# Performance work log

Measured on AMD Instinct MI355X. Metric: run time of the kernel, lower is better.

## Reference

```python
import jax, jax.numpy as jnp
import numpy as np

B, T, C = 1, 3072, 1024
H, KVH, HD = 16, 4, 64
HI, DI = 16, 32
LOCAL = 128
TOP_K = max(int(T * 0.5), LOCAL)  # 1536
EPS = 1.1920929e-07  # torch fp32 finfo eps used by F.rms_norm
NEG = -1.0e9
POS = 1.0e9


def _rope(x, cos, sin):
    d = x.shape[-1] // 2
    x1, x2 = x[..., :d], x[..., d:]
    return jnp.concatenate([x1 * cos + x2 * sin, -x1 * sin + x2 * cos], axis=-1)


def _rms(x):
    return x * jax.lax.rsqrt(jnp.mean(x * x, axis=-1, keepdims=True) + EPS)


def setup_inputs() -> dict:
    key = jax.random.key(0)
    ks = jax.random.split(key, 10)
    s = 0.02
    return {
        "x": jax.random.normal(ks[0], (B, T, C), jnp.float32),
        "cos": jax.random.uniform(ks[1], (1, T, 1, HD // 2), jnp.float32),
        "sin": jax.random.uniform(ks[2], (1, T, 1, HD // 2), jnp.float32),
        "Wq": jax.random.normal(ks[3], (C, H * HD), jnp.float32) * s,
        "Wk": jax.random.normal(ks[4], (C, KVH * HD), jnp.float32) * s,
        "Wv": jax.random.normal(ks[5], (C, KVH * HD), jnp.float32) * s,
        "Wo": jax.random.normal(ks[6], (C, C), jnp.float32) * s,
        "Wiq": jax.random.normal(ks[7], (C, HI * DI), jnp.float32) * s,
        "Wik": jax.random.normal(ks[8], (C, DI), jnp.float32) * s,
        "Wiw": jax.random.normal(ks[9], (C, HI), jnp.float32) * s,
    }


def reference(x, cos, sin, Wq, Wk, Wv, Wo, Wiq, Wik, Wiw):
    # projections
    q = (x @ Wq).reshape(B, T, H, HD)
    k = (x @ Wk).reshape(B, T, KVH, HD)
    v = (x @ Wv).reshape(B, T, KVH, HD)
    q, k = _rope(q, cos, sin), _rope(k, cos, sin)
    q, k = _rms(q), _rms(k)

    # lightning indexer: I(t,s) = sum_h w(t,h) * relu(q_I(t,h).k_I(s))
    iq = (x @ Wiq).reshape(B, T, HI, DI)
    ik = x @ Wik  # (B,T,DI)
    iw = x @ Wiw  # (B,T,HI)
    sc = jax.nn.relu(jnp.einsum('bqhd,bkd->bqhk', iq, ik))
    imp = jnp.einsum('bqh,bqhk->bqk', iw, sc)  # (B,T,T)

    pos = jnp.arange(T)
    causal = (pos[None, :] > pos[:, None])  # True where key s > query t
    dist = pos[None, :] - pos[:, None]
    in_local = (dist >= 0) & (dist < LOCAL)
    imp = jnp.where(causal[None], NEG, imp)
    imp = jnp.where(in_local[None], POS, imp)

    # hard top-k mask
    _, top_idx = jax.lax.top_k(imp, TOP_K)  # (B,T,K)
    bi = jnp.arange(B)[:, None, None]
    ti = jnp.arange(T)[None, :, None]
    hard = jnp.zeros((B, T, T), x.dtype).at[bi, ti, top_idx].set(1.0)
    causal_f = causal.astype(x.dtype)[None]
    hard = hard * (1.0 - causal_f)
    di = jnp.arange(T)
    hard = hard.at[:, di, di].set(1.0)

    # straight-through sigmoid gate
    soft = jax.nn.sigmoid(imp * 0.1) * (1.0 - causal_f)
    soft = soft.at[:, di, di].set(1.0)
    gate = soft + jax.lax.stop_gradient(hard - soft)
    attn_bias = jnp.log(jnp.clip(gate, 1e-6))[:, None]  # (B,1,T,T)

    # GQA attention with additive bias
    rep = H // KVH
    qs = q.transpose(0, 2, 1, 3)                        # (B,H,T,HD)
    ks_ = jnp.repeat(k.transpose(0, 2, 1, 3), rep, axis=1)
    vs = jnp.repeat(v.transpose(0, 2, 1, 3), rep, axis=1)
    scale = 1.0 / np.sqrt(HD)
    logits = jnp.einsum('bhqd,bhkd->bhqk', qs, ks_) * scale + attn_bias
    att = jax.nn.softmax(logits, axis=-1)
    y = jnp.einsum('bhqk,bhkd->bhqd', att, vs)
    y = y.transpose(0, 2, 1, 3).reshape(B, T, C)
    return y @ Wo
```

## Files before the change

kernel.cpp:

```cpp
#include <hip/hip_runtime.h>
#include <hip/hip_bf16.h>
#include <math.h>

#define T_SEQ   3072
#define C_DIM   1024
#define NH      16
#define NKV     4
#define HD      64
#define HI      16
#define DI      32
#define LOCAL_W 128
#define TOPK    1536
#define SELQ0   (TOPK - LOCAL_W + 1)
#define RMS_EPS 1.1920929e-07f
#define LOGEPS  -13.815510558f
#define SCALE   0.125f
#define MASKW   (T_SEQ / 32)
#define QKVI_N  2176
#define IQ_OFF  1536
#define IK_OFF  2048
#define IW_OFF  2080

typedef __bf16 bf16_t;
typedef __bf16 bf16x8 __attribute__((ext_vector_type(8)));
typedef float  f32x4  __attribute__((ext_vector_type(4)));

__global__ __launch_bounds__(256) void transp_conv(const float* __restrict__ W,
                                                   bf16_t* __restrict__ Wt, int N) {
    __shared__ float t[64][65];
    int n0 = blockIdx.x * 64, k0 = blockIdx.y * 64;
#pragma unroll
    for (int it = 0; it < 16; ++it) {
        int flat = it * 256 + threadIdx.x;
        int i = flat >> 6, j = flat & 63;
        t[i][j] = W[(size_t)(k0 + i) * N + n0 + j];
    }
    __syncthreads();
#pragma unroll
    for (int it = 0; it < 16; ++it) {
        int flat = it * 256 + threadIdx.x;
        int n = flat >> 6, kk = flat & 63;
        Wt[(size_t)(n0 + n) * 1024 + k0 + kk] = (bf16_t)t[kk][n];
    }
}

__global__ __launch_bounds__(256) void transp_conv_g(const float* __restrict__ W,
                                                     bf16_t* __restrict__ Wt, int N) {
    __shared__ float t[64][65];
    int k0 = blockIdx.y * 64;
#pragma unroll
    for (int it = 0; it < 16; ++it) {
        int flat = it * 256 + threadIdx.x;
        int i = flat >> 6, j = flat & 63;
        t[i][j] = (j < N) ? W[(size_t)(k0 + i) * N + j] : 0.f;
    }
    __syncthreads();
#pragma unroll
    for (int it = 0; it < 16; ++it) {
        int flat = it * 256 + threadIdx.x;
        int n = flat >> 6, kk = flat & 63;
        if (n < N) Wt[(size_t)n * 1024 + k0 + kk] = (bf16_t)t[kk][n];
    }
}

__global__ __launch_bounds__(256) void pack_kv(const float* __restrict__ qkvi,
                                               bf16_t* __restrict__ Kb,
                                               bf16_t* __restrict__ Vtg) {
    __shared__ float t[64][65];
    int t0 = blockIdx.x * 64, kvh = blockIdx.y;
#pragma unroll
    for (int it = 0; it < 2; ++it) {
        int s = it * 256 + threadIdx.x;
        int row = s >> 3, slot = s & 7;
        const float* src = &qkvi[(size_t)(t0 + row) * QKVI_N + 1024 + kvh * HD + slot * 8];
        float4 a = *reinterpret_cast<const float4*>(src);
        float4 b = *reinterpret_cast<const float4*>(src + 4);
        bf16x8 v;
        v[0] = (bf16_t)a.x; v[1] = (bf16_t)a.y; v[2] = (bf16_t)a.z; v[3] = (bf16_t)a.w;
        v[4] = (bf16_t)b.x; v[5] = (bf16_t)b.y; v[6] = (bf16_t)b.z; v[7] = (bf16_t)b.w;
        *reinterpret_cast<bf16x8*>(&Kb[(size_t)(t0 + row) * (NKV * HD) + kvh * HD + slot * 8]) = v;
    }
#pragma unroll
    for (int it = 0; it < 16; ++it) {
        int flat = it * 256 + threadIdx.x;
        int i = flat >> 6, j = flat & 63;
        t[i][j] = qkvi[(size_t)(t0 + i) * QKVI_N + 1280 + kvh * HD + j];
    }
    __syncthreads();
#pragma unroll
    for (int it = 0; it < 16; ++it) {
        int flat = it * 256 + threadIdx.x;
        int dd = flat >> 6, tt = flat & 63;
        Vtg[(size_t)(kvh * HD + dd) * T_SEQ + t0 + tt] = (bf16_t)t[tt][dd];
    }
}

__global__ __launch_bounds__(256) void causal_mask(unsigned* __restrict__ selm) {
    int idx = blockIdx.x * 256 + threadIdx.x;
    if (idx >= SELQ0 * MASKW) return;
    int row = idx / MASKW, w = idx % MASKW;
    int wq = row >> 5, b = row & 31;
    unsigned v;
    if (w < wq) v = ~0u;
    else if (w == wq) v = (b == 31) ? ~0u : ((1u << (b + 1)) - 1u);
    else v = 0u;
    selm[(size_t)row * MASKW + w] = v;
}

template<bool A_F32>
__global__ __launch_bounds__(256) void gemm_mfma_t(const void* __restrict__ Ap,
                                                   const bf16_t* __restrict__ Bt,
                                                   float* __restrict__ C, int N) {
    __shared__ __align__(16) bf16_t As[128 * 64];
    __shared__ __align__(16) bf16_t Bs[128 * 64];
    const int tid = threadIdx.x;
    const int m0 = blockIdx.y * 128, n0 = blockIdx.x * 128;
    const int wid = tid >> 6, lane = tid & 63;
    const int wr = wid >> 1, wc = wid & 1;
    const int fr = lane & 15, fq = lane >> 4;

    f32x4 acc[4][4];
#pragma unroll
    for (int i = 0; i < 4; ++i)
#pragma unroll
        for (int j = 0; j < 4; ++j) acc[i][j] = (f32x4){0.f, 0.f, 0.f, 0.f};

    for (int k0 = 0; k0 < 1024; k0 += 64) {
        __syncthreads();
#pragma unroll
        for (int s = tid; s < 1024; s += 256) {
            int row = s >> 3, slot = s & 7;
            int sw = slot ^ (row & 7);
            bf16x8 av;
            if constexpr (A_F32) {
                const float* A = (const float*)Ap;
                const float* src = &A[(size_t)(m0 + row) * 1024 + k0 + slot * 8];
                float4 a = *reinterpret_cast<const float4*>(src);
                float4 b = *reinterpret_cast<const float4*>(src + 4);
                av[0] = (bf16_t)a.x; av[1] = (bf16_t)a.y; av[2] = (bf16_t)a.z; av[3] = (bf16_t)a.w;
                av[4] = (bf16_t)b.x; av[5] = (bf16_t)b.y; av[6] = (bf16_t)b.z; av[7] = (bf16_t)b.w;
            } else {
                const bf16_t* A = (const bf16_t*)Ap;
                av = *reinterpret_cast<const bf16x8*>(&A[(size_t)(m0 + row) * 1024 + k0 + slot * 8]);
            }
            *reinterpret_cast<bf16x8*>(&As[row * 64 + sw * 8]) = av;
            bf16x8 bv = *reinterpret_cast<const bf16x8*>(&Bt[(size_t)(n0 + row) * 1024 + k0 + slot * 8]);
            *reinterpret_cast<bf16x8*>(&Bs[row * 64 + sw * 8]) = bv;
        }
        __syncthreads();
#pragma unroll
        for (int kk = 0; kk < 2; ++kk) {
            bf16x8 af[4], bfr[4];
#pragma unroll
            for (int i = 0; i < 4; ++i) {
                int arow = wr * 64 + i * 16 + fr;
                int aslot = (kk * 4 + fq) ^ (arow & 7);
                af[i] = *reinterpret_cast<const bf16x8*>(&As[arow * 64 + aslot * 8]);
                int brow = wc * 64 + i * 16 + fr;
                int bslot = (kk * 4 + fq) ^ (brow & 7);
                bfr[i] = *reinterpret_cast<const bf16x8*>(&Bs[brow * 64 + bslot * 8]);
            }
#pragma unroll
            for (int i = 0; i < 4; ++i)
#pragma unroll
                for (int j = 0; j < 4; ++j)
                    acc[i][j] = __builtin_amdgcn_mfma_f32_16x16x32_bf16(af[i], bfr[j], acc[i][j], 0, 0, 0);
        }
    }
#pragma unroll
    for (int i = 0; i < 4; ++i)
#pragma unroll
        for (int j = 0; j < 4; ++j)
#pragma unroll
            for (int r = 0; r < 4; ++r) {
                int row = m0 + wr * 64 + i * 16 + fq * 4 + r;
                int col = n0 + wc * 64 + j * 16 + fr;
                C[(size_t)row * N + col] = acc[i][j][r];
            }
}

__global__ __launch_bounds__(256) void rope_rms(float* __restrict__ data,
                                                const float* __restrict__ cosb,
                                                const float* __restrict__ sinb,
                                                int nheads, int rowstride, int coloff) {
    int idx = blockIdx.x * blockDim.x + threadIdx.x;
    if (idx >= T_SEQ * nheads) return;
    int t = idx / nheads, hh = idx % nheads;
    float* p = data + (size_t)t * rowstride + coloff + hh * HD;
    float o[HD];
    float ss = 0.f;
#pragma unroll
    for (int d = 0; d < 32; ++d) {
        float x1 = p[d], x2 = p[d + 32];
        float c = cosb[t * 32 + d], s = sinb[t * 32 + d];
        float a = x1 * c + x2 * s;
        float b = x2 * c - x1 * s;
        o[d] = a; o[d + 32] = b;
        ss += a * a + b * b;
    }
    float r = 1.0f / sqrtf(ss * (1.0f / HD) + RMS_EPS);
#pragma unroll
    for (int d = 0; d < HD; ++d) p[d] = o[d] * r;
}

__global__ __launch_bounds__(256) void imp_select(const float* __restrict__ qkvi,
                                                  unsigned* __restrict__ selmask) {
    const int q = SELQ0 + blockIdx.x;
    const int tid = threadIdx.x;
    const int wid = tid >> 6, lane = tid & 63;
    const int fr = lane & 15, fq = lane >> 4;

    __shared__ unsigned keys[T_SEQ];
    __shared__ unsigned hist[256];
    __shared__ int sufx[257];
    __shared__ unsigned gtw[MASKW], eqw[MASKW];
    __shared__ int s_digit, s_need;

    const float* iqp = &qkvi[(size_t)q * QKVI_N + IQ_OFF + fr * DI + fq * 8];
    float4 qa = *reinterpret_cast<const float4*>(iqp);
    float4 qb = *reinterpret_cast<const float4*>(iqp + 4);
    bf16x8 bq;
    bq[0] = (bf16_t)qa.x; bq[1] = (bf16_t)qa.y; bq[2] = (bf16_t)qa.z; bq[3] = (bf16_t)qa.w;
    bq[4] = (bf16_t)qb.x; bq[5] = (bf16_t)qb.y; bq[6] = (bf16_t)qb.z; bq[7] = (bf16_t)qb.w;
    const float wh = qkvi[(size_t)q * QKVI_N + IW_OFF + fr];

    for (int k0 = 0; k0 < q; k0 += 64) {
        int krow = k0 + wid * 16 + fr;
        const float* ikp = &qkvi[(size_t)krow * QKVI_N + IK_OFF + fq * 8];
        float4 a = *reinterpret_cast<const float4*>(ikp);
        float4 b = *reinterpret_cast<const float4*>(ikp + 4);
        bf16x8 ak;
        ak[0] = (bf16_t)a.x; ak[1] = (bf16_t)a.y; ak[2] = (bf16_t)a.z; ak[3] = (bf16_t)a.w;
        ak[4] = (bf16_t)b.x; ak[5] = (bf16_t)b.y; ak[6] = (bf16_t)b.z; ak[7] = (bf16_t)b.w;
        f32x4 c = (f32x4){0.f, 0.f, 0.f, 0.f};
        c = __builtin_amdgcn_mfma_f32_16x16x32_bf16(ak, bq, c, 0, 0, 0);
        float p0 = wh * fmaxf(c[0], 0.f);
        float p1 = wh * fmaxf(c[1], 0.f);
        float p2 = wh * fmaxf(c[2], 0.f);
        float p3 = wh * fmaxf(c[3], 0.f);
#pragma unroll
        for (int m = 1; m < 16; m <<= 1) {
            p0 += __shfl_xor(p0, m);
            p1 += __shfl_xor(p1, m);
            p2 += __shfl_xor(p2, m);
            p3 += __shfl_xor(p3, m);
        }
        if (fr == 0) {
            int kb = k0 + wid * 16 + fq * 4;
            float pv[4] = {p0, p1, p2, p3};
#pragma unroll
            for (int r = 0; r < 4; ++r) {
                int k = kb + r;
                if (k < q) {
                    unsigned u = __float_as_uint(pv[r]);
                    keys[k] = (u & 0x80000000u) ? ~u : (u | 0x80000000u);
                }
            }
        }
    }
    __syncthreads();

    const int F = min(LOCAL_W, T_SEQ - q);
    int need = TOPK - F;
    unsigned pref = 0;
    for (int b = 3; b >= 0; --b) {
        hist[tid] = 0;
        __syncthreads();
        unsigned above = (b == 3) ? 0u : (~0u << ((b + 1) * 8));
        for (int k = tid; k < q; k += 256) {
            unsigned key = keys[k];
            if ((key & above) == (pref & above))
                atomicAdd(&hist[(key >> (b * 8)) & 255u], 1u);
        }
        __syncthreads();
        sufx[tid] = (int)hist[tid];
        if (tid == 0) sufx[256] = 0;
        __syncthreads();
        for (int s = 1; s < 256; s <<= 1) {
            int v = sufx[tid] + ((tid + s < 256) ? sufx[tid + s] : 0);
            __syncthreads();
            sufx[tid] = v;
            __syncthreads();
        }
        int nxt = sufx[tid + 1];
        if (sufx[tid] >= need && nxt < need) { s_digit = tid; s_need = need - nxt; }
        __syncthreads();
        pref |= ((unsigned)s_digit) << (b * 8);
        need = s_need;
        __syncthreads();
    }
    const unsigned V = pref;
    const int slots = need;

    for (int w = tid; w < MASKW; w += 256) {
        unsigned g = 0, e = 0;
        int kbase = w * 32;
#pragma unroll 4
        for (int bit = 0; bit < 32; ++bit) {
            int k = kbase + bit;
            if (k < q) {
                unsigned key = keys[k];
                if (key > V) g |= (1u << bit);
                else if (key == V) e |= (1u << bit);
            }
        }
        gtw[w] = g; eqw[w] = e;
    }
    __syncthreads();
    if (tid == 0) {
        int rem = slots;
        for (int w = 0; w < MASKW && rem > 0; ++w) {
            unsigned e = eqw[w];
            if (!e) continue;
            int pc = __popc(e);
            if (pc <= rem) { gtw[w] |= e; rem -= pc; }
            else {
                unsigned sel = 0;
                for (int i = 0; i < rem; ++i) { unsigned lb = e & (~e + 1u); sel |= lb; e ^= lb; }
                gtw[w] |= sel; rem = 0;
            }
        }
    }
    __syncthreads();
    for (int w = tid; w < MASKW; w += 256) {
        unsigned g = gtw[w];
        if (w == (q >> 5)) g |= (1u << (q & 31));
        selmask[(size_t)q * MASKW + w] = g;
    }
}

__global__ __launch_bounds__(256) void attn_mfma(const float* __restrict__ qkvi,
                                                 const bf16_t* __restrict__ Kb,
                                                 const bf16_t* __restrict__ Vtg,
                                                 const unsigned* __restrict__ selmask,
                                                 float* __restrict__ yb) {
    const int q0 = blockIdx.x * 64;
    const int h = blockIdx.y;
    const int kvh = h >> 2;
    const int tid = threadIdx.x;
    const int wid = tid >> 6, lane = tid & 63;
    const int fr = lane & 15, fq = lane >> 4;

    __shared__ __align__(16) bf16_t Qs[64 * 64];
    __shared__ __align__(16) bf16_t Ks[64 * 64];
    __shared__ __align__(16) bf16_t Vts[64 * 64];
    __shared__ __align__(16) float Sb[64][68];
    __shared__ unsigned mlds[64][2];
    __shared__ float mrow[64], lrow[64], arow[64];

#pragma unroll
    for (int it = 0; it < 2; ++it) {
        int s = it * 256 + tid;
        int row = s >> 3, slot = s & 7;
        const float* src = &qkvi[(size_t)(q0 + row) * QKVI_N + h * HD + slot * 8];
        float4 a = *reinterpret_cast<const float4*>(src);
        float4 b = *reinterpret_cast<const float4*>(src + 4);
        bf16x8 v;
        v[0] = (bf16_t)(a.x * SCALE); v[1] = (bf16_t)(a.y * SCALE);
        v[2] = (bf16_t)(a.z * SCALE); v[3] = (bf16_t)(a.w * SCALE);
        v[4] = (bf16_t)(b.x * SCALE); v[5] = (bf16_t)(b.y * SCALE);
        v[6] = (bf16_t)(b.z * SCALE); v[7] = (bf16_t)(b.w * SCALE);
        *reinterpret_cast<bf16x8*>(&Qs[row * 64 + (slot ^ (row & 7)) * 8]) = v;
    }
    if (tid < 64) { mrow[tid] = -1e30f; lrow[tid] = 0.f; }

    f32x4 oc[4];
#pragma unroll
    for (int j = 0; j < 4; ++j) oc[j] = (f32x4){0.f, 0.f, 0.f, 0.f};
    __syncthreads();

    for (int k0 = 0; k0 < T_SEQ; k0 += 64) {
#pragma unroll
        for (int it = 0; it < 2; ++it) {
            int s = it * 256 + tid;
            int row = s >> 3, slot = s & 7;
            *reinterpret_cast<bf16x8*>(&Ks[row * 64 + (slot ^ (row & 7)) * 8]) =
                *reinterpret_cast<const bf16x8*>(&Kb[(size_t)(k0 + row) * (NKV * HD) + kvh * HD + slot * 8]);
            *reinterpret_cast<bf16x8*>(&Vts[row * 64 + (slot ^ (row & 7)) * 8]) =
                *reinterpret_cast<const bf16x8*>(&Vtg[(size_t)(kvh * HD + row) * T_SEQ + k0 + slot * 8]);
        }
        if (tid < 128) {
            int row = tid >> 1, w = tid & 1;
            mlds[row][w] = selmask[(size_t)(q0 + row) * MASKW + (k0 >> 5) + w];
        }
        __syncthreads();

        f32x4 sacc[4];
#pragma unroll
        for (int j = 0; j < 4; ++j) sacc[j] = (f32x4){0.f, 0.f, 0.f, 0.f};
#pragma unroll
        for (int kc = 0; kc < 2; ++kc) {
            int arow_ = wid * 16 + fr;
            bf16x8 aq = *reinterpret_cast<const bf16x8*>(&Qs[arow_ * 64 + (((kc * 4 + fq) ^ (arow_ & 7))) * 8]);
#pragma unroll
            for (int jb = 0; jb < 4; ++jb) {
                int brow = jb * 16 + fr;
                bf16x8 bk = *reinterpret_cast<const bf16x8*>(&Ks[brow * 64 + (((kc * 4 + fq) ^ (brow & 7))) * 8]);
                sacc[jb] = __builtin_amdgcn_mfma_f32_16x16x32_bf16(aq, bk, sacc[jb], 0, 0, 0);
            }
        }
#pragma unroll
        for (int jb = 0; jb < 4; ++jb)
#pragma unroll
            for (int r = 0; r < 4; ++r) {
                unsigned mw = mlds[wid * 16 + fq * 4 + r][jb >> 1];
                float bias = ((mw >> ((jb & 1) * 16 + fr)) & 1u) ? 0.f : LOGEPS;
                Sb[wid * 16 + fq * 4 + r][jb * 16 + fr] = sacc[jb][r] + bias;
            }
        __syncthreads();

        {
            int r = tid >> 2, ln = tid & 3;
            float4* sp = reinterpret_cast<float4*>(&Sb[r][ln * 16]);
            float4 v0 = sp[0], v1 = sp[1], v2 = sp[2], v3 = sp[3];
            float mx = fmaxf(fmaxf(fmaxf(v0.x, v0.y), fmaxf(v0.z, v0.w)),
                             fmaxf(fmaxf(v1.x, v1.y), fmaxf(v1.z, v1.w)));
            mx = fmaxf(mx, fmaxf(fmaxf(fmaxf(v2.x, v2.y), fmaxf(v2.z, v2.w)),
                                 fmaxf(fmaxf(v3.x, v3.y), fmaxf(v3.z, v3.w))));
            mx = fmaxf(mx, __shfl_xor(mx, 1, 64));
            mx = fmaxf(mx, __shfl_xor(mx, 2, 64));
            float mnew = fmaxf(mrow[r], mx);
            v0.x = __expf(v0.x - mnew); v0.y = __expf(v0.y - mnew);
            v0.z = __expf(v0.z - mnew); v0.w = __expf(v0.w - mnew);
            v1.x = __expf(v1.x - mnew); v1.y = __expf(v1.y - mnew);
            v1.z = __expf(v1.z - mnew); v1.w = __expf(v1.w - mnew);
            v2.x = __expf(v2.x - mnew); v2.y = __expf(v2.y - mnew);
            v2.z = __expf(v2.z - mnew); v2.w = __expf(v2.w - mnew);
            v3.x = __expf(v3.x - mnew); v3.y = __expf(v3.y - mnew);
            v3.z = __expf(v3.z - mnew); v3.w = __expf(v3.w - mnew);
            float ssum = (v0.x + v0.y + v0.z + v0.w) + (v1.x + v1.y + v1.z + v1.w)
                       + (v2.x + v2.y + v2.z + v2.w) + (v3.x + v3.y + v3.z + v3.w);
            sp[0] = v0; sp[1] = v1; sp[2] = v2; sp[3] = v3;
            ssum += __shfl_xor(ssum, 1, 64);
            ssum += __shfl_xor(ssum, 2, 64);
            if (ln == 0) {
                float a = __expf(mrow[r] - mnew);
                lrow[r] = lrow[r] * a + ssum;
                mrow[r] = mnew;
                arow[r] = a;
            }
        }
        __syncthreads();

#pragma unroll
        for (int r = 0; r < 4; ++r) {
            float a = arow[wid * 16 + fq * 4 + r];
#pragma unroll
            for (int jb = 0; jb < 4; ++jb) oc[jb][r] *= a;
        }
#pragma unroll
        for (int kc = 0; kc < 2; ++kc) {
            const float* ps = &Sb[wid * 16 + fr][kc * 32 + fq * 8];
            float4 p0 = *reinterpret_cast<const float4*>(ps);
            float4 p1 = *reinterpret_cast<const float4*>(ps + 4);
            bf16x8 ap;
            ap[0] = (bf16_t)p0.x; ap[1] = (bf16_t)p0.y; ap[2] = (bf16_t)p0.z; ap[3] = (bf16_t)p0.w;
            ap[4] = (bf16_t)p1.x; ap[5] = (bf16_t)p1.y; ap[6] = (bf16_t)p1.z; ap[7] = (bf16_t)p1.w;
#pragma unroll
            for (int jb = 0; jb < 4; ++jb) {
                int brow = jb * 16 + fr;
                bf16x8 bv = *reinterpret_cast<const bf16x8*>(&Vts[brow * 64 + (((kc * 4 + fq) ^ (brow & 7))) * 8]);
                oc[jb] = __builtin_amdgcn_mfma_f32_16x16x32_bf16(ap, bv, oc[jb], 0, 0, 0);
            }
        }
        __syncthreads();
    }

#pragma unroll
    for (int r = 0; r < 4; ++r) {
        int rowl = wid * 16 + fq * 4 + r;
        float inv = 1.0f / lrow[rowl];
#pragma unroll
        for (int jb = 0; jb < 4; ++jb)
            yb[(size_t)(q0 + rowl) * C_DIM + h * HD + jb * 16 + fr] = oc[jb][r] * inv;
    }
}

extern "C" void kernel_launch(void* const* d_in, const int* in_sizes, int n_in,
                              void* d_out, int out_size, void* d_ws, size_t ws_size,
                              hipStream_t stream) {
    const float* x    = (const float*)d_in[0];
    const float* cosb = (const float*)d_in[1];
    const float* sinb = (const float*)d_in[2];
    const float* Wq   = (const float*)d_in[3];
    const float* Wk   = (const float*)d_in[4];
    const float* Wv   = (const float*)d_in[5];
    const float* Wo   = (const float*)d_in[6];
    const float* Wiq  = (const float*)d_in[7];
    const float* Wik  = (const float*)d_in[8];
    const float* Wiw  = (const float*)d_in[9];
    float* out = (float*)d_out;

    char* cur = (char*)d_ws;
    auto carve = [&](size_t bytes) { char* p = cur; cur += (bytes + 255) & ~(size_t)255; return p; };
    float*    qkvi  = (float*)   carve((size_t)T_SEQ * QKVI_N * 4);
    float*    yb    = (float*)   carve((size_t)T_SEQ * C_DIM * 4);
    unsigned* selm  = (unsigned*)carve((size_t)T_SEQ * MASKW * 4);
    bf16_t*   Wtp   = (bf16_t*)  carve((size_t)QKVI_N * C_DIM * 2);
    bf16_t*   Wot   = (bf16_t*)  carve((size_t)C_DIM * C_DIM * 2);
    bf16_t*   Vtg   = (bf16_t*)  carve((size_t)NKV * HD * T_SEQ * 2);
    bf16_t*   Kb16  = (bf16_t*)  carve((size_t)T_SEQ * NKV * HD * 2);
    if ((size_t)(cur - (char*)d_ws) > ws_size) return;

    dim3 blk(256);

    transp_conv<<<dim3(16, 16), blk, 0, stream>>>(Wq,  Wtp + (size_t)0    * 1024, 1024);
    transp_conv<<<dim3(4, 16),  blk, 0, stream>>>(Wk,  Wtp + (size_t)1024 * 1024, 256);
    transp_conv<<<dim3(4, 16),  blk, 0, stream>>>(Wv,  Wtp + (size_t)1280 * 1024, 256);
    transp_conv<<<dim3(8, 16),  blk, 0, stream>>>(Wiq, Wtp + (size_t)IQ_OFF * 1024, 512);
    transp_conv_g<<<dim3(1, 16), blk, 0, stream>>>(Wik, Wtp + (size_t)IK_OFF * 1024, DI);
    transp_conv_g<<<dim3(1, 16), blk, 0, stream>>>(Wiw, Wtp + (size_t)IW_OFF * 1024, HI);
    transp_conv<<<dim3(16, 16), blk, 0, stream>>>(Wo,  Wot, 1024);

    gemm_mfma_t<true><<<dim3(QKVI_N / 128, T_SEQ / 128), blk, 0, stream>>>(x, Wtp, qkvi, QKVI_N);
    causal_mask<<<(SELQ0 * MASKW + 255) / 256, blk, 0, stream>>>(selm);

    rope_rms<<<(T_SEQ * NH + 255) / 256, blk, 0, stream>>>(qkvi, cosb, sinb, NH, QKVI_N, 0);
    rope_rms<<<(T_SEQ * NKV + 255) / 256, blk, 0, stream>>>(qkvi, cosb, sinb, NKV, QKVI_N, 1024);
    pack_kv<<<dim3(T_SEQ / 64, NKV), blk, 0, stream>>>(qkvi, Kb16, Vtg);

    imp_select<<<T_SEQ - SELQ0, blk, 0, stream>>>(qkvi, selm);

    attn_mfma<<<dim3(T_SEQ / 64, NH), blk, 0, stream>>>(qkvi, Kb16, Vtg, selm, yb);

    gemm_mfma_t<true><<<dim3(C_DIM / 128, T_SEQ / 128), blk, 0, stream>>>(yb, Wot, out, C_DIM);
}
```

Measured before the change: 429.7 us.

## Keep attention softmax in registers via transposed S=K·Q MFMA and lane shuffles

The attention kernel now computes scores as K·Q so each lane holds all keys for one query row, which lets it do the online-softmax max and sum in registers with cross-lane shuffles. The shared-memory score buffer, the Q staging buffer, the per-row m/l/alpha arrays and two of the three barriers per tile are removed. The probabilities are packed to bf16 and redistributed with shuffles into the A-operand layout for the P·V MFMA. This adds shuffle traffic and register pressure in exchange for less LDS traffic and fewer synchronisations.

New measurement: 419.6 us. 1.02x faster.

```diff
diff --git a/kernel.cpp b/kernel.cpp
--- a/kernel.cpp
+++ b/kernel.cpp
@@ -25,6 +25,12 @@
 typedef __bf16 bf16x8 __attribute__((ext_vector_type(8)));
 typedef float  f32x4  __attribute__((ext_vector_type(4)));
 
+static __device__ inline unsigned packbf(float a, float b) {
+    union { bf16_t h[2]; unsigned u; } cv;
+    cv.h[0] = (bf16_t)a; cv.h[1] = (bf16_t)b;
+    return cv.u;
+}
+
 __global__ __launch_bounds__(256) void transp_conv(const float* __restrict__ W,
                                                    bf16_t* __restrict__ Wt, int N) {
     __shared__ float t[64][65];
@@ -341,35 +347,33 @@
     const int wid = tid >> 6, lane = tid & 63;
     const int fr = lane & 15, fq = lane >> 4;
 
-    __shared__ __align__(16) bf16_t Qs[64 * 64];
     __shared__ __align__(16) bf16_t Ks[64 * 64];
     __shared__ __align__(16) bf16_t Vts[64 * 64];
-    __shared__ __align__(16) float Sb[64][68];
     __shared__ unsigned mlds[64][2];
-    __shared__ float mrow[64], lrow[64], arow[64];
-
-#pragma unroll
-    for (int it = 0; it < 2; ++it) {
-        int s = it * 256 + tid;
-        int row = s >> 3, slot = s & 7;
-        const float* src = &qkvi[(size_t)(q0 + row) * QKVI_N + h * HD + slot * 8];
-        float4 a = *reinterpret_cast<const float4*>(src);
-        float4 b = *reinterpret_cast<const float4*>(src + 4);
-        bf16x8 v;
-        v[0] = (bf16_t)(a.x * SCALE); v[1] = (bf16_t)(a.y * SCALE);
-        v[2] = (bf16_t)(a.z * SCALE); v[3] = (bf16_t)(a.w * SCALE);
-        v[4] = (bf16_t)(b.x * SCALE); v[5] = (bf16_t)(b.y * SCALE);
-        v[6] = (bf16_t)(b.z * SCALE); v[7] = (bf16_t)(b.w * SCALE);
-        *reinterpret_cast<bf16x8*>(&Qs[row * 64 + (slot ^ (row & 7)) * 8]) = v;
-    }
-    if (tid < 64) { mrow[tid] = -1e30f; lrow[tid] = 0.f; }
-
+
+    bf16x8 qf[2];
+    {
+        const float* qsrc = &qkvi[(size_t)(q0 + wid * 16 + fr) * QKVI_N + h * HD];
+#pragma unroll
+        for (int kc = 0; kc < 2; ++kc) {
+            float4 a = *reinterpret_cast<const float4*>(qsrc + kc * 32 + fq * 8);
+            float4 b = *reinterpret_cast<const float4*>(qsrc + kc * 32 + fq * 8 + 4);
+            bf16x8 v;
+            v[0] = (bf16_t)(a.x * SCALE); v[1] = (bf16_t)(a.y * SCALE);
+            v[2] = (bf16_t)(a.z * SCALE); v[3] = (bf16_t)(a.w * SCALE);
+            v[4] = (bf16_t)(b.x * SCALE); v[5] = (bf16_t)(b.y * SCALE);
+            v[6] = (bf16_t)(b.z * SCALE); v[7] = (bf16_t)(b.w * SCALE);
+            qf[kc] = v;
+        }
+    }
+
+    float m_reg = -1e30f, l_reg = 0.f;
     f32x4 oc[4];
 #pragma unroll
     for (int j = 0; j < 4; ++j) oc[j] = (f32x4){0.f, 0.f, 0.f, 0.f};
-    __syncthreads();
 
     for (int k0 = 0; k0 < T_SEQ; k0 += 64) {
+        __syncthreads();
 #pragma unroll
         for (int it = 0; it < 2; ++it) {
             int s = it * 256 + tid;
@@ -390,89 +394,94 @@
         for (int j = 0; j < 4; ++j) sacc[j] = (f32x4){0.f, 0.f, 0.f, 0.f};
 #pragma unroll
         for (int kc = 0; kc < 2; ++kc) {
-            int arow_ = wid * 16 + fr;
-            bf16x8 aq = *reinterpret_cast<const bf16x8*>(&Qs[arow_ * 64 + (((kc * 4 + fq) ^ (arow_ & 7))) * 8]);
 #pragma unroll
             for (int jb = 0; jb < 4; ++jb) {
-                int brow = jb * 16 + fr;
-                bf16x8 bk = *reinterpret_cast<const bf16x8*>(&Ks[brow * 64 + (((kc * 4 + fq) ^ (brow & 7))) * 8]);
-                sacc[jb] = __builtin_amdgcn_mfma_f32_16x16x32_bf16(aq, bk, sacc[jb], 0, 0, 0);
-            }
-        }
+                int arow = jb * 16 + fr;
+                bf16x8 ak = *reinterpret_cast<const bf16x8*>(&Ks[arow * 64 + (((kc * 4 + fq) ^ (arow & 7))) * 8]);
+                sacc[jb] = __builtin_amdgcn_mfma_f32_16x16x32_bf16(ak, qf[kc], sacc[jb], 0, 0, 0);
+            }
+        }
+
+        unsigned mw0 = mlds[wid * 16 + fr][0];
+        unsigned mw1 = mlds[wid * 16 + fr][1];
+        float p[4][4];
+        float mx = -1e30f;
+#pragma unroll
+        for (int jb = 0; jb < 4; ++jb) {
+            unsigned mw = (jb & 2) ? mw1 : mw0;
+#pragma unroll
+            for (int r = 0; r < 4; ++r) {
+                float bias = ((mw >> ((jb & 1) * 16 + 4 * fq + r)) & 1u) ? 0.f : LOGEPS;
+                p[jb][r] = sacc[jb][r] + bias;
+                mx = fmaxf(mx, p[jb][r]);
+            }
+        }
+        mx = fmaxf(mx, __shfl_xor(mx, 16, 64));
+        mx = fmaxf(mx, __shfl_xor(mx, 32, 64));
+        float mnew = fmaxf(m_reg, mx);
+        float aold = __expf(m_reg - mnew);
+        float ssum = 0.f;
 #pragma unroll
         for (int jb = 0; jb < 4; ++jb)
 #pragma unroll
             for (int r = 0; r < 4; ++r) {
-                unsigned mw = mlds[wid * 16 + fq * 4 + r][jb >> 1];
-                float bias = ((mw >> ((jb & 1) * 16 + fr)) & 1u) ? 0.f : LOGEPS;
-                Sb[wid * 16 + fq * 4 + r][jb * 16 + fr] = sacc[jb][r] + bias;
-            }
-        __syncthreads();
-
-        {
-            int r = tid >> 2, ln = tid & 3;
-            float4* sp = reinterpret_cast<float4*>(&Sb[r][ln * 16]);
-            float4 v0 = sp[0], v1 = sp[1], v2 = sp[2], v3 = sp[3];
-            float mx = fmaxf(fmaxf(fmaxf(v0.x, v0.y), fmaxf(v0.z, v0.w)),
-                             fmaxf(fmaxf(v1.x, v1.y), fmaxf(v1.z, v1.w)));
-            mx = fmaxf(mx, fmaxf(fmaxf(fmaxf(v2.x, v2.y), fmaxf(v2.z, v2.w)),
-                                 fmaxf(fmaxf(v3.x, v3.y), fmaxf(v3.z, v3.w))));
-            mx = fmaxf(mx, __shfl_xor(mx, 1, 64));
-            mx = fmaxf(mx, __shfl_xor(mx, 2, 64));
-            float mnew = fmaxf(mrow[r], mx);
-            v0.x = __expf(v0.x - mnew); v0.y = __expf(v0.y - mnew);
-            v0.z = __expf(v0.z - mnew); v0.w = __expf(v0.w - mnew);
-            v1.x = __expf(v1.x - mnew); v1.y = __expf(v1.y - mnew);
-            v1.z = __expf(v1.z - mnew); v1.w = __expf(v1.w - mnew);
-            v2.x = __expf(v2.x - mnew); v2.y = __expf(v2.y - mnew);
-            v2.z = __expf(v2.z - mnew); v2.w = __expf(v2.w - mnew);
-            v3.x = __expf(v3.x - mnew); v3.y = __expf(v3.y - mnew);
-            v3.z = __expf(v3.z - mnew); v3.w = __expf(v3.w - mnew);
-            float ssum = (v0.x + v0.y + v0.z + v0.w) + (v1.x + v1.y + v1.z + v1.w)
-                       + (v2.x + v2.y + v2.z + v2.w) + (v3.x + v3.y + v3.z + v3.w);
-            sp[0] = v0; sp[1] = v1; sp[2] = v2; sp[3] = v3;
-            ssum += __shfl_xor(ssum, 1, 64);
-            ssum += __shfl_xor(ssum, 2, 64);
-            if (ln == 0) {
-                float a = __expf(mrow[r] - mnew);
-                lrow[r] = lrow[r] * a + ssum;
-                mrow[r] = mnew;
-                arow[r] = a;
-            }
-        }
-        __syncthreads();
-
-#pragma unroll
-        for (int r = 0; r < 4; ++r) {
-            float a = arow[wid * 16 + fq * 4 + r];
-#pragma unroll
-            for (int jb = 0; jb < 4; ++jb) oc[jb][r] *= a;
-        }
+                p[jb][r] = __expf(p[jb][r] - mnew);
+                ssum += p[jb][r];
+            }
+        ssum += __shfl_xor(ssum, 16, 64);
+        ssum += __shfl_xor(ssum, 32, 64);
+        l_reg = l_reg * aold + ssum;
+        m_reg = mnew;
+
+        unsigned w32[4][2];
+#pragma unroll
+        for (int jb = 0; jb < 4; ++jb) {
+            w32[jb][0] = packbf(p[jb][0], p[jb][1]);
+            w32[jb][1] = packbf(p[jb][2], p[jb][3]);
+        }
+
+        unsigned n32[2][4];
+#pragma unroll
+        for (int kc = 0; kc < 2; ++kc)
+#pragma unroll
+            for (int jp = 0; jp < 4; ++jp) {
+                int src = fr + 16 * (2 * (fq & 1) + (jp >> 1));
+                unsigned lo = __shfl(w32[2 * kc][jp & 1], src, 64);
+                unsigned hi = __shfl(w32[2 * kc + 1][jp & 1], src, 64);
+                n32[kc][jp] = (fq >> 1) ? hi : lo;
+            }
+
+        float a4[4];
+#pragma unroll
+        for (int r = 0; r < 4; ++r) a4[r] = __shfl(aold, 4 * fq + r, 64);
+#pragma unroll
+        for (int jb = 0; jb < 4; ++jb)
+#pragma unroll
+            for (int r = 0; r < 4; ++r) oc[jb][r] *= a4[r];
+
 #pragma unroll
         for (int kc = 0; kc < 2; ++kc) {
-            const float* ps = &Sb[wid * 16 + fr][kc * 32 + fq * 8];
-            float4 p0 = *reinterpret_cast<const float4*>(ps);
-            float4 p1 = *reinterpret_cast<const float4*>(ps + 4);
-            bf16x8 ap;
-            ap[0] = (bf16_t)p0.x; ap[1] = (bf16_t)p0.y; ap[2] = (bf16_t)p0.z; ap[3] = (bf16_t)p0.w;
-            ap[4] = (bf16_t)p1.x; ap[5] = (bf16_t)p1.y; ap[6] = (bf16_t)p1.z; ap[7] = (bf16_t)p1.w;
+            union { unsigned u[4]; bf16x8 v; } cv;
+            cv.u[0] = n32[kc][0]; cv.u[1] = n32[kc][1];
+            cv.u[2] = n32[kc][2]; cv.u[3] = n32[kc][3];
 #pragma unroll
             for (int jb = 0; jb < 4; ++jb) {
                 int brow = jb * 16 + fr;
                 bf16x8 bv = *reinterpret_cast<const bf16x8*>(&Vts[brow * 64 + (((kc * 4 + fq) ^ (brow & 7))) * 8]);
-                oc[jb] = __builtin_amdgcn_mfma_f32_16x16x32_bf16(ap, bv, oc[jb], 0, 0, 0);
-            }
-        }
-        __syncthreads();
-    }
-
+                oc[jb] = __builtin_amdgcn_mfma_f32_16x16x32_bf16(cv.v, bv, oc[jb], 0, 0, 0);
+            }
+        }
+    }
+
+    float inv4[4];
+#pragma unroll
+    for (int r = 0; r < 4; ++r) inv4[r] = 1.0f / __shfl(l_reg, 4 * fq + r, 64);
 #pragma unroll
     for (int r = 0; r < 4; ++r) {
         int rowl = wid * 16 + fq * 4 + r;
-        float inv = 1.0f / lrow[rowl];
 #pragma unroll
         for (int jb = 0; jb < 4; ++jb)
-            yb[(size_t)(q0 + rowl) * C_DIM + h * HD + jb * 16 + fr] = oc[jb][r] * inv;
+            yb[(size_t)(q0 + rowl) * C_DIM + h * HD + jb * 16 + fr] = oc[jb][r] * inv4[r];
     }
 }
 
```
